# Performance work log

Hardware: AMD Instinct MI355X
Metric: run time of the kernel (lower is better)

## Reference

```python
import jax, jax.numpy as jnp
import numpy as np

N_HEADS = 16


def setup_inputs() -> dict:
    key = jax.random.key(0)
    k1, k2, k3 = jax.random.split(key, 3)
    b, t, d = 2, 2048, 1024
    x = jax.random.normal(k1, (b, t, d), dtype=jnp.float32)
    # nn.Linear weights (stored here as [in, out]); 0.02 scale ~ standard init
    w_qkv = jax.random.normal(k2, (d, 3 * d), dtype=jnp.float32) * 0.02
    w_out = jax.random.normal(k3, (d, d), dtype=jnp.float32) * 0.02
    return {"x": x, "w_qkv": w_qkv, "w_out": w_out}


def reference(x, w_qkv, w_out):
    # Causal multi-head self-attention. The original module implements this
    # via a hand-rolled blockwise flash-attention loop with online softmax;
    # the intended math is exactly standard causal SDPA, expressed densely here.
    b, t, d = x.shape
    h = N_HEADS
    hd = d // h
    qkv = (x @ w_qkv).reshape(b, t, 3, h, hd)
    qkv = jnp.transpose(qkv, (2, 0, 3, 1, 4))  # [3, b, h, t, hd]
    q, k, v = qkv[0], qkv[1], qkv[2]
    scale = 1.0 / jnp.sqrt(jnp.float32(hd))
    s = jnp.einsum("bhqd,bhkd->bhqk", q, k) * scale  # [b, h, t, t]
    causal = jnp.tril(jnp.ones((t, t), dtype=bool))
    s = jnp.where(causal, s, -jnp.inf)
    p = jax.nn.softmax(s, axis=-1)
    o = jnp.einsum("bhqk,bhkd->bhqd", p, v)
    o = jnp.transpose(o, (0, 2, 1, 3)).reshape(b, t, d)
    return o @ w_out
```

## Files before the change

### kernel.cpp

```cpp
#include <hip/hip_runtime.h>

typedef float f32x4 __attribute__((ext_vector_type(4)));
typedef short short8 __attribute__((ext_vector_type(8)));
typedef short short4_t __attribute__((ext_vector_type(4)));

#define GLOAD_LDS16(gp, lp) \
  __builtin_amdgcn_global_load_lds((const __attribute__((address_space(1))) void*)(gp), \
                                   (__attribute__((address_space(3))) void*)(lp), 16, 0, 0)

__device__ __forceinline__ short f2bf(float f){
  unsigned u = __builtin_bit_cast(unsigned, f);
  u += 0x7fffu + ((u >> 16) & 1u);
  return (short)(u >> 16);
}

__device__ __forceinline__ float exp2_fast(float x){
  return __builtin_amdgcn_exp2f(x);
}

__global__ void cvt_kernel(const float* __restrict__ x, short* __restrict__ xb, int n4){
  for (int i = blockIdx.x*blockDim.x + threadIdx.x; i < n4; i += gridDim.x*blockDim.x){
    f32x4 v = ((const f32x4*)x)[i];
    short4_t s;
    s[0]=f2bf(v[0]); s[1]=f2bf(v[1]); s[2]=f2bf(v[2]); s[3]=f2bf(v[3]);
    ((short4_t*)xb)[i] = s;
  }
}

__global__ __launch_bounds__(256) void transpose_cvt_kernel(const float* __restrict__ w,
                                                            short* __restrict__ wT,
                                                            int K, int N){
  __shared__ float tile[32][33];
  int bn = blockIdx.x*32, bk = blockIdx.y*32;
  int tx = threadIdx.x & 31, ty = threadIdx.x >> 5;
  #pragma unroll
  for (int r=ty; r<32; r+=8) tile[r][tx] = w[(size_t)(bk+r)*N + bn + tx];
  __syncthreads();
  #pragma unroll
  for (int r=ty; r<32; r+=8) wT[(size_t)(bn+r)*K + bk + tx] = f2bf(tile[tx][r]);
}

template<int MODE>
__global__ __launch_bounds__(256) void gemm128_kernel(
    const short* __restrict__ A, const short* __restrict__ Bt,
    float* __restrict__ Cf, short* __restrict__ qb_, short* __restrict__ kb_,
    short* __restrict__ vtb, int M, int N, int K)
{
  __shared__ short a_lds[128*64];
  __shared__ short b_lds[128*64];
  const int tid = threadIdx.x;
  const int lane = tid & 63;
  const int l15 = lane & 15, lg = lane >> 4;
  const int w  = tid >> 6;
  const int wr = w >> 1, wc = w & 1;
  const int m0 = blockIdx.x * 128, n0 = blockIdx.y * 128;

  f32x4 acc[4][4];
  #pragma unroll
  for (int i=0;i<4;i++)
    #pragma unroll
    for (int j=0;j<4;j++) acc[i][j] = (f32x4){0.f,0.f,0.f,0.f};

  for (int kt = 0; kt < K; kt += 64){
    __syncthreads();
    #pragma unroll
    for (int i=0;i<4;i++){
      int u = i*256 + tid;
      int row = u >> 3, cu = u & 7;
      int kl = ((cu ^ (row & 7)) << 3);
      GLOAD_LDS16(A + (size_t)(m0+row)*K + kt + kl, a_lds + (size_t)(i*256 + (tid & ~63))*8);
    }
    #pragma unroll
    for (int i=0;i<4;i++){
      int u = i*256 + tid;
      int row = u >> 3, cu = u & 7;
      int kl = ((cu ^ (row & 7)) << 3);
      GLOAD_LDS16(Bt + (size_t)(n0+row)*K + kt + kl, b_lds + (size_t)(i*256 + (tid & ~63))*8);
    }
    asm volatile("s_waitcnt vmcnt(0)" ::: "memory");
    __syncthreads();

    #pragma unroll
    for (int kk=0;kk<2;kk++){
      short8 af[4], bfr[4];
      #pragma unroll
      for (int mi=0;mi<4;mi++){
        int row = wr*64 + mi*16 + l15;
        int uu = ((kk*4 + lg) ^ (row & 7));
        af[mi] = *(const short8*)&a_lds[row*64 + uu*8];
      }
      #pragma unroll
      for (int ni=0;ni<4;ni++){
        int row = wc*64 + ni*16 + l15;
        int uu = ((kk*4 + lg) ^ (row & 7));
        bfr[ni] = *(const short8*)&b_lds[row*64 + uu*8];
      }
      #pragma unroll
      for (int mi=0;mi<4;mi++)
        #pragma unroll
        for (int ni=0;ni<4;ni++)
          acc[mi][ni] = __builtin_amdgcn_mfma_f32_16x16x32_bf16(af[mi], bfr[ni], acc[mi][ni], 0,0,0);
    }
  }

  #pragma unroll
  for (int mi=0;mi<4;mi++){
    #pragma unroll
    for (int ni=0;ni<4;ni++){
      int col = n0 + wc*64 + ni*16 + l15;
      #pragma unroll
      for (int r=0;r<4;r++){
        int rowg = m0 + wr*64 + mi*16 + lg*4 + r;
        float v = acc[mi][ni][r];
        if (MODE == 0){
          Cf[(size_t)rowg*N + col] = v;
        } else {
          int three = col >> 10, hh = (col >> 6) & 15, e = col & 63;
          int bb = rowg >> 11, t = rowg & 2047;
          int bh = bb*16 + hh;
          if (three == 0)      qb_[((size_t)bh*2048 + t)*64 + e] = f2bf(v * (0.125f*1.44269504f));
          else if (three == 1) kb_[((size_t)bh*2048 + t)*64 + e] = f2bf(v);
          else                 vtb[((size_t)bh*64 + e)*2048 + t] = f2bf(v);
        }
      }
    }
  }
}

__global__ __launch_bounds__(512) void attn_kernel(
    const short* __restrict__ q, const short* __restrict__ kbuf,
    const short* __restrict__ vt, short* __restrict__ ob)
{
  __shared__ short k_lds[2][64*64];
  __shared__ short v_lds[2][64*64];
  __shared__ short p_lds[8*16*72];

  const int tid = threadIdx.x, lane = tid & 63, w = tid >> 6;
  const int l15 = lane & 15, lg = lane >> 4;
  const int qi = blockIdx.x >> 5;
  const int qb = (qi < 8) ? (15 - qi) : (qi - 8);
  const int bh = blockIdx.x & 31;
  const int q0 = qb * 128;

  const short* qg = q + ((size_t)bh*2048 + q0 + w*16 + l15)*64;
  short8 qf[2];
  qf[0] = *(const short8*)(qg + lg*8);
  qf[1] = *(const short8*)(qg + 32 + lg*8);

  f32x4 o_acc[4];
  #pragma unroll
  for (int ct=0;ct<4;ct++) o_acc[ct] = (f32x4){0.f,0.f,0.f,0.f};
  float mreg = -1e30f, lreg = 0.f;

  int rdo[2][4];
  #pragma unroll
  for (int kk=0;kk<2;kk++)
    #pragma unroll
    for (int ct=0;ct<4;ct++){
      int row = ct*16 + l15;
      int uu = (kk*4 + lg) ^ (row & 7);
      rdo[kk][ct] = (row*64 + uu*8)*2;
    }

  const int grow = tid >> 3, gcu = tid & 7;
  const int gkl = ((gcu ^ (grow & 7)) << 3);
  const short* kp = kbuf + (size_t)bh*2048*64 + (size_t)grow*64   + gkl;
  const short* vp = vt   + (size_t)bh*64*2048 + (size_t)grow*2048 + gkl;
  const int wbase = (tid & ~63)*8;

  char* pw = (char*)(p_lds + w*16*72);
  const int pwo = (l15*72 + lg*4)*2;
  const int pro = (l15*72 + lg*8)*2;

  const int n = 2*qb + 2;
  GLOAD_LDS16(kp, &k_lds[0][wbase]); kp += 4096;
  GLOAD_LDS16(vp, &v_lds[0][wbase]); vp += 64;

  for (int s = 0; s < n; s++){
    const int cur = s & 1;
    if (s + 1 < n){
      GLOAD_LDS16(kp, &k_lds[cur^1][wbase]); kp += 4096;
      GLOAD_LDS16(vp, &v_lds[cur^1][wbase]); vp += 64;
      asm volatile("s_waitcnt vmcnt(2)" ::: "memory");
    } else {
      asm volatile("s_waitcnt vmcnt(0)" ::: "memory");
    }
    __builtin_amdgcn_s_barrier();

    const char* kl_ = (const char*)&k_lds[cur][0];
    const char* vl_ = (const char*)&v_lds[cur][0];

    f32x4 sacc[4];
    #pragma unroll
    for (int ct=0;ct<4;ct++) sacc[ct] = (f32x4){0.f,0.f,0.f,0.f};
    #pragma unroll
    for (int kk=0;kk<2;kk++){
      #pragma unroll
      for (int ct=0;ct<4;ct++){
        short8 kf = *(const short8*)(kl_ + rdo[kk][ct]);
        sacc[ct] = __builtin_amdgcn_mfma_f32_16x16x32_bf16(kf, qf[kk], sacc[ct], 0,0,0);
      }
    }

    if (s >= 2*qb){
      int d = s - 2*qb;
      int qloc = w*16 + l15;
      #pragma unroll
      for (int ct=0;ct<4;ct++){
        #pragma unroll
        for (int r=0;r<4;r++)
          if (d*64 + ct*16 + lg*4 + r > qloc) sacc[ct][r] = -1e30f;
      }
    }

    float m01 = fmaxf(fmaxf(sacc[0][0], sacc[0][1]), fmaxf(sacc[0][2], sacc[0][3]));
    float m23 = fmaxf(fmaxf(sacc[1][0], sacc[1][1]), fmaxf(sacc[1][2], sacc[1][3]));
    float m45 = fmaxf(fmaxf(sacc[2][0], sacc[2][1]), fmaxf(sacc[2][2], sacc[2][3]));
    float m67 = fmaxf(fmaxf(sacc[3][0], sacc[3][1]), fmaxf(sacc[3][2], sacc[3][3]));
    float mx = fmaxf(fmaxf(m01, m23), fmaxf(m45, m67));
    mx = fmaxf(mx, __shfl_xor(mx, 16));
    mx = fmaxf(mx, __shfl_xor(mx, 32));
    float mnew = fmaxf(mreg, mx);
    float alpha = exp2_fast(mreg - mnew);
    mreg = mnew;

    f32x4 p[4];
    float sum = 0.f;
    #pragma unroll
    for (int ct=0;ct<4;ct++)
      #pragma unroll
      for (int r=0;r<4;r++){
        p[ct][r] = exp2_fast(sacc[ct][r] - mnew);
        sum += p[ct][r];
      }
    sum += __shfl_xor(sum, 16);
    sum += __shfl_xor(sum, 32);
    lreg = lreg*alpha + sum;

    float alphaRow[4];
    #pragma unroll
    for (int r=0;r<4;r++) alphaRow[r] = __shfl(alpha, lg*4 + r);
    #pragma unroll
    for (int ct=0;ct<4;ct++)
      #pragma unroll
      for (int r=0;r<4;r++) o_acc[ct][r] *= alphaRow[r];

    #pragma unroll
    for (int ct=0;ct<4;ct++){
      uint2 pk;
      asm("v_cvt_pk_bf16_f32 %0, %1, %2" : "=v"(pk.x) : "v"(p[ct][0]), "v"(p[ct][1]));
      asm("v_cvt_pk_bf16_f32 %0, %1, %2" : "=v"(pk.y) : "v"(p[ct][2]), "v"(p[ct][3]));
      *(uint2*)(pw + pwo + ct*32) = pk;
    }
    asm volatile("s_waitcnt lgkmcnt(0)" ::: "memory");

    #pragma unroll
    for (int kh=0;kh<2;kh++){
      short8 pa = *(const short8*)(pw + pro + kh*64);
      #pragma unroll
      for (int ct=0;ct<4;ct++){
        short8 vf = *(const short8*)(vl_ + rdo[kh][ct]);
        o_acc[ct] = __builtin_amdgcn_mfma_f32_16x16x32_bf16(pa, vf, o_acc[ct], 0,0,0);
      }
    }

    __builtin_amdgcn_s_barrier();
  }

  int bb = bh >> 4, hh = bh & 15;
  float lfin[4];
  #pragma unroll
  for (int r=0;r<4;r++) lfin[r] = __shfl(lreg, lg*4 + r);
  #pragma unroll
  for (int r=0;r<4;r++){
    float inv = 1.0f / lfin[r];
    int t = q0 + w*16 + lg*4 + r;
    size_t base = ((size_t)(bb*2048 + t))*1024 + (size_t)hh*64;
    #pragma unroll
    for (int ct=0;ct<4;ct++)
      ob[base + ct*16 + l15] = f2bf(o_acc[ct][r] * inv);
  }
}

extern "C" void kernel_launch(void* const* d_in, const int* in_sizes, int n_in,
                              void* d_out, int out_size, void* d_ws, size_t ws_size,
                              hipStream_t stream) {
  const float* x     = (const float*)d_in[0];
  const float* w_qkv = (const float*)d_in[1];
  const float* w_out = (const float*)d_in[2];
  float* out = (float*)d_out;

  char* ws = (char*)d_ws;
  short* xb    = (short*)(ws);
  short* wqkvT = (short*)(ws + (8u  << 20));
  short* woutT = (short*)(ws + (14u << 20));
  short* qbuf  = (short*)(ws + (16u << 20));
  short* kbuf  = (short*)(ws + (24u << 20));
  short* vtbuf = (short*)(ws + (32u << 20));
  short* obuf  = (short*)(ws + (40u << 20));

  cvt_kernel<<<2048, 256, 0, stream>>>(x, xb, (4096*1024)/4);
  transpose_cvt_kernel<<<dim3(96,32), 256, 0, stream>>>(w_qkv, wqkvT, 1024, 3072);
  transpose_cvt_kernel<<<dim3(32,32), 256, 0, stream>>>(w_out, woutT, 1024, 1024);

  gemm128_kernel<1><<<dim3(32,24), 256, 0, stream>>>(xb, wqkvT, nullptr,
                                                     qbuf, kbuf, vtbuf, 4096, 3072, 1024);
  attn_kernel<<<dim3(512), 512, 0, stream>>>(qbuf, kbuf, vtbuf, obuf);
  gemm128_kernel<0><<<dim3(32,8), 256, 0, stream>>>(obuf, woutT, out,
                                                    nullptr, nullptr, nullptr, 4096, 1024, 1024);
}
```

Baseline: 118.8 us.

## Rewrite attention kernel with 32x32 MFMA, 128-key tiles and register-resident P

Reworks the attention kernel so each of 4 waves owns 32 query rows and uses 32x32x16 bf16 MFMA, processing 128-key tiles per step instead of 64. The probability matrix no longer round-trips through LDS; it is rearranged in registers with v_permlane32_swap and fed directly as the MFMA A operand. It also adds lazy rescaling that skips the running-max update when the max grows by at most 8, plus s_setprio around MFMA sections. This cuts LDS traffic, per-tile overhead and rescale work, at the cost of higher register pressure and fewer threads per block.

```diff
diff --git a/kernel.cpp b/kernel.cpp
--- a/kernel.cpp
+++ b/kernel.cpp
@@ -1,6 +1,7 @@
 #include <hip/hip_runtime.h>
 
 typedef float f32x4 __attribute__((ext_vector_type(4)));
+typedef float f32x16 __attribute__((ext_vector_type(16)));
 typedef short short8 __attribute__((ext_vector_type(8)));
 typedef short short4_t __attribute__((ext_vector_type(4)));
 
@@ -127,61 +128,61 @@
   }
 }
 
-__global__ __launch_bounds__(512) void attn_kernel(
+__global__ __launch_bounds__(256) void attn_kernel(
     const short* __restrict__ q, const short* __restrict__ kbuf,
     const short* __restrict__ vt, short* __restrict__ ob)
 {
-  __shared__ short k_lds[2][64*64];
-  __shared__ short v_lds[2][64*64];
-  __shared__ short p_lds[8*16*72];
+  __shared__ short k_lds[2][128*64];
+  __shared__ short v_lds[2][64*128];
 
   const int tid = threadIdx.x, lane = tid & 63, w = tid >> 6;
-  const int l15 = lane & 15, lg = lane >> 4;
+  const int l31 = lane & 31, hi = lane >> 5;
   const int qi = blockIdx.x >> 5;
   const int qb = (qi < 8) ? (15 - qi) : (qi - 8);
   const int bh = blockIdx.x & 31;
   const int q0 = qb * 128;
 
-  const short* qg = q + ((size_t)bh*2048 + q0 + w*16 + l15)*64;
-  short8 qf[2];
-  qf[0] = *(const short8*)(qg + lg*8);
-  qf[1] = *(const short8*)(qg + 32 + lg*8);
-
-  f32x4 o_acc[4];
-  #pragma unroll
-  for (int ct=0;ct<4;ct++) o_acc[ct] = (f32x4){0.f,0.f,0.f,0.f};
+  const short* qg = q + ((size_t)bh*2048 + q0 + w*32 + l31)*64 + hi*8;
+  short8 qf[4];
+  #pragma unroll
+  for (int kk=0;kk<4;kk++) qf[kk] = *(const short8*)(qg + kk*16);
+
+  f32x16 o_acc[2];
+  #pragma unroll
+  for (int oc=0;oc<2;oc++)
+    #pragma unroll
+    for (int r=0;r<16;r++) o_acc[oc][r] = 0.f;
   float mreg = -1e30f, lreg = 0.f;
 
-  int rdo[2][4];
-  #pragma unroll
-  for (int kk=0;kk<2;kk++)
-    #pragma unroll
-    for (int ct=0;ct<4;ct++){
-      int row = ct*16 + l15;
-      int uu = (kk*4 + lg) ^ (row & 7);
-      rdo[kk][ct] = (row*64 + uu*8)*2;
-    }
-
-  const int grow = tid >> 3, gcu = tid & 7;
-  const int gkl = ((gcu ^ (grow & 7)) << 3);
-  const short* kp = kbuf + (size_t)bh*2048*64 + (size_t)grow*64   + gkl;
-  const short* vp = vt   + (size_t)bh*64*2048 + (size_t)grow*2048 + gkl;
-  const int wbase = (tid & ~63)*8;
-
-  char* pw = (char*)(p_lds + w*16*72);
-  const int pwo = (l15*72 + lg*4)*2;
-  const int pro = (l15*72 + lg*8)*2;
-
-  const int n = 2*qb + 2;
-  GLOAD_LDS16(kp, &k_lds[0][wbase]); kp += 4096;
-  GLOAD_LDS16(vp, &v_lds[0][wbase]); vp += 64;
+  const int sw = l31 & 7;
+  int kro[4], vro[8];
+  #pragma unroll
+  for (int kk=0;kk<4;kk++) kro[kk] = l31*128 + (((kk*2+hi)^sw) << 4);
+  #pragma unroll
+  for (int ks=0;ks<8;ks++) vro[ks] = l31*256 + (((ks*2+hi)^sw) << 4);
+
+  const int xk = ((tid & 7) ^ ((tid >> 3) & 7)) * 8;
+  const int xv = ((tid & 15) ^ ((tid >> 4) & 7)) * 8;
+  const short* kp = kbuf + (size_t)bh*2048*64 + (size_t)(tid >> 3)*64 + xk;
+  const short* vp = vt   + (size_t)bh*64*2048 + (size_t)(tid >> 4)*2048 + xv;
+  const int dst = (tid & ~63)*8;
+
+  const int n = qb + 1;
+  #pragma unroll
+  for (int i=0;i<4;i++) GLOAD_LDS16(kp + i*2048,  &k_lds[0][i*2048 + dst]);
+  #pragma unroll
+  for (int i=0;i<4;i++) GLOAD_LDS16(vp + i*32768, &v_lds[0][i*2048 + dst]);
+  kp += 8192; vp += 128;
 
   for (int s = 0; s < n; s++){
     const int cur = s & 1;
     if (s + 1 < n){
-      GLOAD_LDS16(kp, &k_lds[cur^1][wbase]); kp += 4096;
-      GLOAD_LDS16(vp, &v_lds[cur^1][wbase]); vp += 64;
-      asm volatile("s_waitcnt vmcnt(2)" ::: "memory");
+      #pragma unroll
+      for (int i=0;i<4;i++) GLOAD_LDS16(kp + i*2048,  &k_lds[cur^1][i*2048 + dst]);
+      #pragma unroll
+      for (int i=0;i<4;i++) GLOAD_LDS16(vp + i*32768, &v_lds[cur^1][i*2048 + dst]);
+      kp += 8192; vp += 128;
+      asm volatile("s_waitcnt vmcnt(8)" ::: "memory");
     } else {
       asm volatile("s_waitcnt vmcnt(0)" ::: "memory");
     }
@@ -190,95 +191,95 @@
     const char* kl_ = (const char*)&k_lds[cur][0];
     const char* vl_ = (const char*)&v_lds[cur][0];
 
-    f32x4 sacc[4];
-    #pragma unroll
-    for (int ct=0;ct<4;ct++) sacc[ct] = (f32x4){0.f,0.f,0.f,0.f};
-    #pragma unroll
-    for (int kk=0;kk<2;kk++){
+    f32x16 sacc[4];
+    #pragma unroll
+    for (int ct=0;ct<4;ct++)
+      #pragma unroll
+      for (int r=0;r<16;r++) sacc[ct][r] = 0.f;
+    __builtin_amdgcn_s_setprio(1);
+    #pragma unroll
+    for (int kk=0;kk<4;kk++){
       #pragma unroll
       for (int ct=0;ct<4;ct++){
-        short8 kf = *(const short8*)(kl_ + rdo[kk][ct]);
-        sacc[ct] = __builtin_amdgcn_mfma_f32_16x16x32_bf16(kf, qf[kk], sacc[ct], 0,0,0);
-      }
-    }
-
-    if (s >= 2*qb){
-      int d = s - 2*qb;
-      int qloc = w*16 + l15;
-      #pragma unroll
-      for (int ct=0;ct<4;ct++){
+        short8 kf = *(const short8*)(kl_ + kro[kk] + ct*4096);
+        sacc[ct] = __builtin_amdgcn_mfma_f32_32x32x16_bf16(kf, qf[kk], sacc[ct], 0,0,0);
+      }
+    }
+    __builtin_amdgcn_s_setprio(0);
+
+    if (s == qb){
+      const int qloc = w*32 + l31 - 4*hi;
+      #pragma unroll
+      for (int ct=0;ct<4;ct++)
         #pragma unroll
-        for (int r=0;r<4;r++)
-          if (d*64 + ct*16 + lg*4 + r > qloc) sacc[ct][r] = -1e30f;
-      }
-    }
-
-    float m01 = fmaxf(fmaxf(sacc[0][0], sacc[0][1]), fmaxf(sacc[0][2], sacc[0][3]));
-    float m23 = fmaxf(fmaxf(sacc[1][0], sacc[1][1]), fmaxf(sacc[1][2], sacc[1][3]));
-    float m45 = fmaxf(fmaxf(sacc[2][0], sacc[2][1]), fmaxf(sacc[2][2], sacc[2][3]));
-    float m67 = fmaxf(fmaxf(sacc[3][0], sacc[3][1]), fmaxf(sacc[3][2], sacc[3][3]));
-    float mx = fmaxf(fmaxf(m01, m23), fmaxf(m45, m67));
-    mx = fmaxf(mx, __shfl_xor(mx, 16));
-    mx = fmaxf(mx, __shfl_xor(mx, 32));
-    float mnew = fmaxf(mreg, mx);
-    float alpha = exp2_fast(mreg - mnew);
-    mreg = mnew;
-
-    f32x4 p[4];
+        for (int r=0;r<16;r++)
+          if (ct*32 + (r&3) + 8*(r>>2) > qloc) sacc[ct][r] = -1e30f;
+    }
+
+    float pmax = sacc[0][0];
+    #pragma unroll
+    for (int ct=0;ct<4;ct++)
+      #pragma unroll
+      for (int r=0;r<16;r++) pmax = fmaxf(pmax, sacc[ct][r]);
+    pmax = fmaxf(pmax, __shfl_xor(pmax, 32));
+
+    if (!__all(pmax - mreg <= 8.0f)){
+      float mnew = fmaxf(mreg, pmax);
+      float alpha = exp2_fast(mreg - mnew);
+      mreg = mnew;
+      lreg *= alpha;
+      float aRow[16];
+      #pragma unroll
+      for (int r=0;r<16;r++) aRow[r] = __shfl(alpha, (r&3) + 8*(r>>2) + 4*hi);
+      #pragma unroll
+      for (int oc=0;oc<2;oc++)
+        #pragma unroll
+        for (int r=0;r<16;r++) o_acc[oc][r] *= aRow[r];
+    }
+
     float sum = 0.f;
     #pragma unroll
-    for (int ct=0;ct<4;ct++)
-      #pragma unroll
-      for (int r=0;r<4;r++){
-        p[ct][r] = exp2_fast(sacc[ct][r] - mnew);
-        sum += p[ct][r];
-      }
-    sum += __shfl_xor(sum, 16);
+    for (int ct=0;ct<4;ct++){
+      float pv[16];
+      #pragma unroll
+      for (int r=0;r<16;r++){ pv[r] = exp2_fast(sacc[ct][r] - mreg); sum += pv[r]; }
+      unsigned pk[8];
+      #pragma unroll
+      for (int t=0;t<8;t++)
+        asm("v_cvt_pk_bf16_f32 %0, %1, %2" : "=v"(pk[t]) : "v"(pv[2*t]), "v"(pv[2*t+1]));
+      #pragma unroll
+      for (int kss=0;kss<2;kss++){
+        const int W = 4*kss;
+        unsigned x0 = pk[W],   x2 = pk[W+2];
+        unsigned x1 = pk[W+1], x3 = pk[W+3];
+        asm("v_permlane32_swap_b32 %0, %1" : "+v"(x0), "+v"(x2));
+        asm("v_permlane32_swap_b32 %0, %1" : "+v"(x1), "+v"(x3));
+        uint4 pau = {x0, x1, x2, x3};
+        short8 pa = __builtin_bit_cast(short8, pau);
+        __builtin_amdgcn_s_setprio(1);
+        #pragma unroll
+        for (int oc=0;oc<2;oc++){
+          short8 vf = *(const short8*)(vl_ + vro[2*ct+kss] + oc*8192);
+          o_acc[oc] = __builtin_amdgcn_mfma_f32_32x32x16_bf16(pa, vf, o_acc[oc], 0,0,0);
+        }
+        __builtin_amdgcn_s_setprio(0);
+      }
+    }
     sum += __shfl_xor(sum, 32);
-    lreg = lreg*alpha + sum;
-
-    float alphaRow[4];
-    #pragma unroll
-    for (int r=0;r<4;r++) alphaRow[r] = __shfl(alpha, lg*4 + r);
-    #pragma unroll
-    for (int ct=0;ct<4;ct++)
-      #pragma unroll
-      for (int r=0;r<4;r++) o_acc[ct][r] *= alphaRow[r];
-
-    #pragma unroll
-    for (int ct=0;ct<4;ct++){
-      uint2 pk;
-      asm("v_cvt_pk_bf16_f32 %0, %1, %2" : "=v"(pk.x) : "v"(p[ct][0]), "v"(p[ct][1]));
-      asm("v_cvt_pk_bf16_f32 %0, %1, %2" : "=v"(pk.y) : "v"(p[ct][2]), "v"(p[ct][3]));
-      *(uint2*)(pw + pwo + ct*32) = pk;
-    }
-    asm volatile("s_waitcnt lgkmcnt(0)" ::: "memory");
-
-    #pragma unroll
-    for (int kh=0;kh<2;kh++){
-      short8 pa = *(const short8*)(pw + pro + kh*64);
-      #pragma unroll
-      for (int ct=0;ct<4;ct++){
-        short8 vf = *(const short8*)(vl_ + rdo[kh][ct]);
-        o_acc[ct] = __builtin_amdgcn_mfma_f32_16x16x32_bf16(pa, vf, o_acc[ct], 0,0,0);
-      }
-    }
+    lreg += sum;
 
     __builtin_amdgcn_s_barrier();
   }
 
-  int bb = bh >> 4, hh = bh & 15;
-  float lfin[4];
-  #pragma unroll
-  for (int r=0;r<4;r++) lfin[r] = __shfl(lreg, lg*4 + r);
-  #pragma unroll
-  for (int r=0;r<4;r++){
-    float inv = 1.0f / lfin[r];
-    int t = q0 + w*16 + lg*4 + r;
-    size_t base = ((size_t)(bb*2048 + t))*1024 + (size_t)hh*64;
-    #pragma unroll
-    for (int ct=0;ct<4;ct++)
-      ob[base + ct*16 + l15] = f2bf(o_acc[ct][r] * inv);
+  const int bb = bh >> 4, hh = bh & 15;
+  #pragma unroll
+  for (int r=0;r<16;r++){
+    float lf = __shfl(lreg, (r&3) + 8*(r>>2) + 4*hi);
+    float inv = 1.0f / lf;
+    int t = q0 + w*32 + (r&3) + 8*(r>>2) + 4*hi;
+    size_t base = ((size_t)(bb*2048 + t))*1024 + (size_t)hh*64 + l31;
+    ob[base]      = f2bf(o_acc[0][r] * inv);
+    ob[base + 32] = f2bf(o_acc[1][r] * inv);
   }
 }
 
@@ -305,7 +306,7 @@
 
   gemm128_kernel<1><<<dim3(32,24), 256, 0, stream>>>(xb, wqkvT, nullptr,
                                                      qbuf, kbuf, vtbuf, 4096, 3072, 1024);
-  attn_kernel<<<dim3(512), 512, 0, stream>>>(qbuf, kbuf, vtbuf, obuf);
+  attn_kernel<<<dim3(512), 256, 0, stream>>>(qbuf, kbuf, vtbuf, obuf);
   gemm128_kernel<0><<<dim3(32,8), 256, 0, stream>>>(obuf, woutT, out,
                                                     nullptr, nullptr, nullptr, 4096, 1024, 1024);
 }
```

Result: no change. 117.2 us (-1.4%).
